# Optimization experiments

Measured on AMD Instinct MI355X. Metric: run time of the kernel, lower is better.

The kernel has to match this reference:

```python
import jax, jax.numpy as jnp
import numpy as np

ALPHA = 0.2          # LeakyReLU negative slope
NEG_INF = -9e15      # mask value used by the original module


def setup_inputs() -> dict:
    key = jax.random.key(0)
    k1, k2, k3, k4 = jax.random.split(key, 4)
    N, C, F, H, E = 4096, 512, 64, 8, 131072
    x = jax.random.normal(k1, (N, C), dtype=jnp.float32)
    edge_index = jax.random.randint(k2, (2, E), 0, N, dtype=jnp.int64)
    # xavier_uniform with gain=1.414 (per-head params stacked on leading axis)
    lim_W = 1.414 * np.sqrt(6.0 / (C + F))
    lim_a = 1.414 * np.sqrt(6.0 / (2 * F + 1))
    W = jax.random.uniform(k3, (H, C, F), minval=-lim_W, maxval=lim_W, dtype=jnp.float32)
    a = jax.random.uniform(k4, (H, 2 * F, 1), minval=-lim_a, maxval=lim_a, dtype=jnp.float32)
    return {"x": x, "edge_index": edge_index, "W": W, "a": a}


def reference(x, edge_index, W, a):
    # x: [N, C]; edge_index: [2, E]; W: [H, C, F]; a: [H, 2F, 1]
    N = x.shape[0]
    H, C, F = W.shape
    # dense adjacency with self-loops (duplicate edges collapse to True, matching adj > 0)
    adj = jnp.zeros((N, N), dtype=bool).at[edge_index[0], edge_index[1]].set(True)
    diag = jnp.arange(N)
    adj = adj.at[diag, diag].set(True)
    # per-head projection: h[h_, i] = x_i @ W[h_]
    h = jnp.einsum('nc,hcf->hnf', x, W)                       # [H, N, F]
    # e_ij = leakyrelu(h_i . a[:F] + h_j . a[F:]) -- identical math to the
    # original's NxN pairwise concat, without materializing [N*N, 2F]
    a_src = a[:, :F, 0]                                        # [H, F]
    a_dst = a[:, F:, 0]                                        # [H, F]
    s_src = jnp.einsum('hnf,hf->hn', h, a_src)                 # [H, N]
    s_dst = jnp.einsum('hnf,hf->hn', h, a_dst)                 # [H, N]
    e = s_src[:, :, None] + s_dst[:, None, :]                  # [H, N, N]
    e = jnp.where(e > 0, e, ALPHA * e)                         # LeakyReLU
    e = jnp.where(adj[None, :, :], e, NEG_INF)                 # mask non-edges
    att = jax.nn.softmax(e, axis=-1)                           # row softmax (dropout=0 / eval)
    out = jnp.einsum('hij,hjf->hif', att, h)                   # [H, N, F]
    out = jnp.transpose(out, (1, 0, 2)).reshape(N, H * F)      # concat heads
    return jax.nn.softmax(out, axis=1)
```

## Files before the change

kernel.cpp:

```cpp
#include <hip/hip_runtime.h>

#define ALPHA 0.2f

typedef __attribute__((ext_vector_type(8))) short short8;
typedef __attribute__((ext_vector_type(8))) unsigned short ushort8;
typedef __attribute__((ext_vector_type(4))) float f32x4;

__device__ __forceinline__ float bf2f(unsigned short u) {
    return __uint_as_float(((unsigned int)u) << 16);
}
__device__ __forceinline__ unsigned short f2bf(float f) {
    unsigned int x = __float_as_uint(f);
    unsigned int r = (x + 0x7fffu + ((x >> 16) & 1u)) >> 16;
    return (unsigned short)r;
}

__device__ __forceinline__ int detect_is32(const unsigned int* xw) {
    int lane = threadIdx.x & 63;
    unsigned int u = xw[lane];
    unsigned int e = (u >> 7) & 0xffu;
    unsigned long long b = __ballot(e >= 0x58u && e <= 0x90u);
    return (__popcll(b) < 40) ? 1 : 0;
}

__global__ __launch_bounds__(256) void split_bf16(const void* __restrict__ x_raw,
                                                  const void* __restrict__ W_raw,
                                                  unsigned short* __restrict__ x_hi,
                                                  unsigned short* __restrict__ x_lo,
                                                  unsigned short* __restrict__ wt_hi,
                                                  unsigned short* __restrict__ wt_lo,
                                                  int* __restrict__ flags) {
    int bid = blockIdx.x, tid = threadIdx.x;
    int is32 = detect_is32((const unsigned int*)x_raw);
    if (bid == 0 && tid == 0) flags[0] = is32;

    if (bid < 1024) {
        size_t base = ((size_t)bid * 256 + tid) * 8;
        ushort8 h8, l8;
        if (is32) {
            const float* xf = (const float*)x_raw;
            float4 v0 = *(const float4*)(xf + base);
            float4 v1 = *(const float4*)(xf + base + 4);
            float v[8] = {v0.x, v0.y, v0.z, v0.w, v1.x, v1.y, v1.z, v1.w};
#pragma unroll
            for (int j = 0; j < 8; j++) {
                unsigned short hi = f2bf(v[j]);
                h8[j] = hi;
                l8[j] = f2bf(v[j] - bf2f(hi));
            }
        } else {
            const ushort8* xb = (const ushort8*)x_raw;
            h8 = xb[base / 8];
            l8 = (ushort8)0;
        }
        *(ushort8*)(x_hi + base) = h8;
        *(ushort8*)(x_lo + base) = l8;
    } else {
        size_t u = ((size_t)(bid - 1024) * 256 + tid) * 8;
#pragma unroll
        for (int j = 0; j < 8; j++) {
            size_t e = u + j;
            int head = (int)(e >> 15);
            int c = (int)((e >> 6) & 511);
            int f = (int)(e & 63);
            unsigned short hi, lo;
            if (is32) {
                float v = ((const float*)W_raw)[e];
                hi = f2bf(v);
                lo = f2bf(v - bf2f(hi));
            } else {
                hi = ((const unsigned short*)W_raw)[e];
                lo = 0;
            }
            size_t o = (size_t)head * 32768 + (size_t)f * 512 + c;
            wt_hi[o] = hi;
            wt_lo[o] = lo;
        }
    }
}

__global__ __launch_bounds__(256) void build_adj(const int* __restrict__ ei, int E, int N,
                                                 unsigned long long* __restrict__ adj) {
    int lane = threadIdx.x & 63;
    unsigned long long nz = __ballot(ei[2 * lane + 1] != 0);
    int is64 = (nz == 0ull) ? 1 : 0;

    int t = blockIdx.x * blockDim.x + threadIdx.x;
    int words = N >> 6;
    if (t < E) {
        int r = is64 ? ei[2 * t]       : ei[t];
        int c = is64 ? ei[2 * (E + t)] : ei[E + t];
        atomicOr(&adj[(size_t)r * words + (c >> 6)], 1ull << (c & 63));
    } else if (t < E + N) {
        int i = t - E;
        atomicOr(&adj[(size_t)i * words + (i >> 6)], 1ull << (i & 63));
    }
}

#define LROW 72
__global__ __launch_bounds__(256) void gemm_mfma(const unsigned short* __restrict__ xh,
                                                 const unsigned short* __restrict__ xl,
                                                 const unsigned short* __restrict__ wth,
                                                 const unsigned short* __restrict__ wtl,
                                                 const void* __restrict__ a_raw,
                                                 unsigned short* __restrict__ h2b,
                                                 float* __restrict__ s_src2,
                                                 float* __restrict__ s_dst2,
                                                 const int* __restrict__ flags) {
    __shared__ unsigned short sA[2][64 * LROW];
    __shared__ unsigned short sB[2][64 * LROW];

    int head = blockIdx.y;
    int row0 = blockIdx.x * 64;
    int tid = threadIdx.x;
    int w = tid >> 6, lane = tid & 63;
    int m = lane & 15, quad = lane >> 4;
    int srow = tid >> 2, sc = tid & 3;

    const unsigned short* Ap[3] = {xh, xl, xh};
    const unsigned short* Bp[3] = {wth, wth, wtl};
    size_t baseA = (size_t)(row0 + srow) * 512 + sc * 8;
    size_t baseB = (size_t)head * 32768 + (size_t)srow * 512 + sc * 8;

    int ldsw  = srow * LROW + sc * 8;
    int ldsAr = (w * 16 + m) * LROW + quad * 8;

    f32x4 acc[4] = {f32x4{0.f, 0.f, 0.f, 0.f}, f32x4{0.f, 0.f, 0.f, 0.f},
                    f32x4{0.f, 0.f, 0.f, 0.f}, f32x4{0.f, 0.f, 0.f, 0.f}};

#define LOADSET(Aa, Ab, Ba, Bb, c)                                         \
    {                                                                      \
        const unsigned short* pA = Ap[(c) >> 3];                           \
        const unsigned short* pB = Bp[(c) >> 3];                           \
        size_t ko = (size_t)((c) & 7) * 64;                                \
        Aa = *(const ushort8*)(pA + baseA + ko);                           \
        Ab = *(const ushort8*)(pA + baseA + ko + 32);                      \
        Ba = *(const ushort8*)(pB + baseB + ko);                           \
        Bb = *(const ushort8*)(pB + baseB + ko + 32);                      \
    }

#define WRITESET(buf, Aa, Ab, Ba, Bb)                                      \
    {                                                                      \
        *(ushort8*)&sA[buf][ldsw]      = Aa;                               \
        *(ushort8*)&sA[buf][ldsw + 32] = Ab;                               \
        *(ushort8*)&sB[buf][ldsw]      = Ba;                               \
        *(ushort8*)&sB[buf][ldsw + 32] = Bb;                               \
    }

#define COMPUTE(buf)                                                       \
    {                                                                      \
        short8 af0 = *(const short8*)&sA[buf][ldsAr];                      \
        short8 af1 = *(const short8*)&sA[buf][ldsAr + 32];                 \
        _Pragma("unroll")                                                  \
        for (int t = 0; t < 4; t++) {                                      \
            int bo = (t * 16 + m) * LROW + quad * 8;                       \
            short8 bf0 = *(const short8*)&sB[buf][bo];                     \
            short8 bf1 = *(const short8*)&sB[buf][bo + 32];                \
            acc[t] = __builtin_amdgcn_mfma_f32_16x16x32_bf16(af0, bf0, acc[t], 0, 0, 0); \
            acc[t] = __builtin_amdgcn_mfma_f32_16x16x32_bf16(af1, bf1, acc[t], 0, 0, 0); \
        }                                                                  \
    }

    ushort8 a0a, a0b, b0a, b0b;
    ushort8 a1a, a1b, b1a, b1b;

    LOADSET(a0a, a0b, b0a, b0b, 0)
    LOADSET(a1a, a1b, b1a, b1b, 1)
    WRITESET(0, a0a, a0b, b0a, b0b)
    __syncthreads();

    for (int i = 0; i < 24; i += 2) {
        if (i + 2 < 24) LOADSET(a0a, a0b, b0a, b0b, i + 2)
        COMPUTE(0)
        WRITESET(1, a1a, a1b, b1a, b1b)
        __syncthreads();
        if (i + 3 < 24) LOADSET(a1a, a1b, b1a, b1b, i + 3)
        COMPUTE(1)
        if (i + 2 < 24) WRITESET(0, a0a, a0b, b0a, b0b)
        __syncthreads();
    }

#pragma unroll
    for (int t = 0; t < 4; t++)
#pragma unroll
        for (int reg = 0; reg < 4; reg++) {
            int r = row0 + w * 16 + quad * 4 + reg;
            h2b[(size_t)r * 512 + head * 64 + t * 16 + m] = f2bf(acc[t][reg]);
        }

    float as[4], ad[4];
    if (flags[0]) {
        const float* af32 = (const float*)a_raw + head * 128;
#pragma unroll
        for (int t = 0; t < 4; t++) {
            as[t] = af32[t * 16 + m];
            ad[t] = af32[64 + t * 16 + m];
        }
    } else {
        const unsigned short* ab = (const unsigned short*)a_raw + head * 128;
#pragma unroll
        for (int t = 0; t < 4; t++) {
            as[t] = bf2f(ab[t * 16 + m]);
            ad[t] = bf2f(ab[64 + t * 16 + m]);
        }
    }
#pragma unroll
    for (int reg = 0; reg < 4; reg++) {
        float s1 = as[0] * acc[0][reg] + as[1] * acc[1][reg] + as[2] * acc[2][reg] + as[3] * acc[3][reg];
        float s2 = ad[0] * acc[0][reg] + ad[1] * acc[1][reg] + ad[2] * acc[2][reg] + ad[3] * acc[3][reg];
#pragma unroll
        for (int d = 1; d < 16; d <<= 1) {
            s1 += __shfl_xor(s1, d);
            s2 += __shfl_xor(s2, d);
        }
        if (m == 0) {
            int r = row0 + w * 16 + quad * 4 + reg;
            s_src2[(size_t)r * 8 + head] = s1;
            s_dst2[(size_t)r * 8 + head] = s2;
        }
    }
}

__global__ __launch_bounds__(256) void attn_out(const unsigned short* __restrict__ h2b,
                                                const float* __restrict__ s_src2,
                                                const float* __restrict__ s_dst2,
                                                const unsigned long long* __restrict__ adj,
                                                void* __restrict__ out_raw,
                                                const int* __restrict__ flags) {
    __shared__ unsigned short nbrs[4096];
    __shared__ float w_lds[256 * 8];
    __shared__ float sss[8], smax[8], sden[8];
    __shared__ float sredw[4][8];
    __shared__ float sr[8];
    __shared__ int s_cnt;

    int i = blockIdx.x;
    int tid = threadIdx.x;
    int lane = tid & 63, wid = tid >> 6;

    if (tid < 64) {
        unsigned long long word = adj[(size_t)i * 64 + tid];
        int cnt = __popcll(word);
        int incl = cnt;
#pragma unroll
        for (int d = 1; d < 64; d <<= 1) {
            int v = __shfl_up(incl, d);
            if (tid >= d) incl += v;
        }
        int off = incl - cnt;
        unsigned long long w = word;
        int base = tid * 64;
        while (w) {
            int b = __ffsll((unsigned long long)w) - 1;
            nbrs[off++] = (unsigned short)(base + b);
            w &= w - 1;
        }
        if (tid == 63) s_cnt = incl;
    }
    if (tid >= 64 && tid < 72) sss[tid - 64] = s_src2[(size_t)i * 8 + (tid - 64)];
    __syncthreads();
    int cnt = s_cnt;

    int hw = tid & 7;
    float mp = -1e30f;
    for (int t = tid; t < cnt * 8; t += 256)
        mp = fmaxf(mp, s_dst2[(size_t)nbrs[t >> 3] * 8 + hw]);
    mp = fmaxf(mp, __shfl_down(mp, 32));
    mp = fmaxf(mp, __shfl_down(mp, 16));
    mp = fmaxf(mp, __shfl_down(mp, 8));
    if (lane < 8) sredw[wid][lane] = mp;
    __syncthreads();
    if (tid < 8) {
        float m = fmaxf(fmaxf(sredw[0][tid], sredw[1][tid]), fmaxf(sredw[2][tid], sredw[3][tid]));
        float pre = sss[tid] + m;
        smax[tid] = pre > 0.f ? pre : ALPHA * pre;
    }
    __syncthreads();

    int hh = tid >> 5;
    float ssrc_w = sss[hw], maxe_w = smax[hw];
    float den = 0.f, ax = 0.f, ay = 0.f;
    for (int c0 = 0; c0 < cnt; c0 += 256) {
        int csz = min(256, cnt - c0);
        __syncthreads();
        for (int t = tid; t < csz * 8; t += 256) {
            int j = nbrs[c0 + (t >> 3)];
            float e = ssrc_w + s_dst2[(size_t)j * 8 + hw];
            e = e > 0.f ? e : ALPHA * e;
            float w = __expf(e - maxe_w);
            w_lds[t] = w;
            den += w;
        }
        __syncthreads();
#pragma unroll 2
        for (int jj = 0; jj < csz; jj++) {
            int j = nbrs[c0 + jj];
            unsigned int u = *(const unsigned int*)(h2b + (size_t)j * 512 + tid * 2);
            float w = w_lds[jj * 8 + hh];
            ax += w * bf2f((unsigned short)(u & 0xffffu));
            ay += w * bf2f((unsigned short)(u >> 16));
        }
    }

    den += __shfl_down(den, 32);
    den += __shfl_down(den, 16);
    den += __shfl_down(den, 8);
    if (lane < 8) sredw[wid][lane] = den;
    __syncthreads();
    if (tid < 8) sden[tid] = sredw[0][tid] + sredw[1][tid] + sredw[2][tid] + sredw[3][tid];
    __syncthreads();
    float dtot = sden[hh];
    float o0 = ax / dtot, o1 = ay / dtot;

    float m2 = fmaxf(o0, o1);
#pragma unroll
    for (int d = 32; d; d >>= 1) m2 = fmaxf(m2, __shfl_down(m2, d));
    if (lane == 0) sr[wid] = m2;
    __syncthreads();
    float m = fmaxf(fmaxf(sr[0], sr[1]), fmaxf(sr[2], sr[3]));
    float e0 = __expf(o0 - m), e1 = __expf(o1 - m);
    float s = e0 + e1;
#pragma unroll
    for (int d = 32; d; d >>= 1) s += __shfl_down(s, d);
    __syncthreads();
    if (lane == 0) sr[wid + 4] = s;
    __syncthreads();
    s = sr[4] + sr[5] + sr[6] + sr[7];

    if (flags[0]) {
        float2* out = (float2*)out_raw;
        out[(size_t)i * 256 + tid] = make_float2(e0 / s, e1 / s);
    } else {
        unsigned int* out = (unsigned int*)out_raw;
        out[(size_t)i * 256 + tid] = (unsigned int)f2bf(e0 / s) | ((unsigned int)f2bf(e1 / s) << 16);
    }
}

extern "C" void kernel_launch(void* const* d_in, const int* in_sizes, int n_in,
                              void* d_out, int out_size, void* d_ws, size_t ws_size,
                              hipStream_t stream) {
    const int N = 4096, H = 8;
    const int E = in_sizes[1] / 2;

    const void* x = d_in[0];
    const int*  ei = (const int*)d_in[1];
    const void* W = d_in[2];
    const void* a = d_in[3];

    char* ws = (char*)d_ws;
    unsigned short* h2b = (unsigned short*)ws;
    float* s_src2 = (float*)(ws + (size_t)4 * 1024 * 1024);
    float* s_dst2 = s_src2 + (size_t)N * H;
    unsigned long long* adj = (unsigned long long*)(ws + (size_t)5 * 1024 * 1024);
    int* flags = (int*)(ws + (size_t)7 * 1024 * 1024 + 512 * 1024);
    unsigned short* x_hi  = (unsigned short*)(ws + (size_t)8 * 1024 * 1024);
    unsigned short* x_lo  = (unsigned short*)(ws + (size_t)12 * 1024 * 1024);
    unsigned short* wt_hi = (unsigned short*)(ws + (size_t)16 * 1024 * 1024);
    unsigned short* wt_lo = (unsigned short*)(ws + (size_t)16 * 1024 * 1024 + 512 * 1024);

    hipMemsetAsync(adj, 0, (size_t)N * (N / 8), stream);

    split_bf16<<<1152, 256, 0, stream>>>(x, W, x_hi, x_lo, wt_hi, wt_lo, flags);
    build_adj<<<(E + N + 255) / 256, 256, 0, stream>>>(ei, E, N, adj);
    gemm_mfma<<<dim3(N / 64, H), 256, 0, stream>>>(x_hi, x_lo, wt_hi, wt_lo, a,
                                                   h2b, s_src2, s_dst2, flags);
    attn_out<<<N, 256, 0, stream>>>(h2b, s_src2, s_dst2, adj, d_out, flags);
}
```

Baseline: 118.7 us.

## Split GEMM K across waves with 64x64 per-wave tiles; use global max for softmax

The GEMM now gives each wave a full 64x64 output tile over a quarter of the K chunks, with per-wave LDS buffers and no block barriers in the main loop. The partial tiles are reduced through LDS at the end, and the attention scores are computed from the reduced tile. The per-row neighbour max pass in attn_out is replaced by a per-head global max of s_dst, gathered with an encoded atomicMax in the GEMM epilogue. This removes a gather pass and two barriers per row. The cost is a looser softmax shift, which is mathematically valid but could hurt numerical range, plus extra registers and LDS in the GEMM.

```diff
diff --git a/kernel.cpp b/kernel.cpp
--- a/kernel.cpp
+++ b/kernel.cpp
@@ -13,6 +13,14 @@
     unsigned int x = __float_as_uint(f);
     unsigned int r = (x + 0x7fffu + ((x >> 16) & 1u)) >> 16;
     return (unsigned short)r;
+}
+__device__ __forceinline__ unsigned int encf(float f) {
+    int i = __float_as_int(f);
+    return (unsigned int)(i ^ ((i >> 31) | 0x80000000));
+}
+__device__ __forceinline__ float decf(unsigned int u) {
+    int i = (int)((u & 0x80000000u) ? (u ^ 0x80000000u) : ~u);
+    return __int_as_float(i);
 }
 
 __device__ __forceinline__ int detect_is32(const unsigned int* xw) {
@@ -33,6 +41,7 @@
     int bid = blockIdx.x, tid = threadIdx.x;
     int is32 = detect_is32((const unsigned int*)x_raw);
     if (bid == 0 && tid == 0) flags[0] = is32;
+    if (bid == 0 && tid >= 8 && tid < 16) flags[tid] = 0;
 
     if (bid < 1024) {
         size_t base = ((size_t)bid * 256 + tid) * 8;
@@ -97,128 +106,144 @@
     }
 }
 
-#define LROW 72
-__global__ __launch_bounds__(256) void gemm_mfma(const unsigned short* __restrict__ xh,
-                                                 const unsigned short* __restrict__ xl,
-                                                 const unsigned short* __restrict__ wth,
-                                                 const unsigned short* __restrict__ wtl,
-                                                 const void* __restrict__ a_raw,
-                                                 unsigned short* __restrict__ h2b,
-                                                 float* __restrict__ s_src2,
-                                                 float* __restrict__ s_dst2,
-                                                 const int* __restrict__ flags) {
-    __shared__ unsigned short sA[2][64 * LROW];
-    __shared__ unsigned short sB[2][64 * LROW];
+#define LR 36
+__global__ __launch_bounds__(256, 2) void gemm_mfma(const unsigned short* __restrict__ xh,
+                                                    const unsigned short* __restrict__ xl,
+                                                    const unsigned short* __restrict__ wth,
+                                                    const unsigned short* __restrict__ wtl,
+                                                    const void* __restrict__ a_raw,
+                                                    unsigned short* __restrict__ h2b,
+                                                    float* __restrict__ s_src2,
+                                                    float* __restrict__ s_dst2,
+                                                    int* __restrict__ flags) {
+    __shared__ unsigned short sbuf[4][2][2][64 * LR];
 
     int head = blockIdx.y;
     int row0 = blockIdx.x * 64;
     int tid = threadIdx.x;
     int w = tid >> 6, lane = tid & 63;
     int m = lane & 15, quad = lane >> 4;
-    int srow = tid >> 2, sc = tid & 3;
+    int srow = lane >> 2, skc = lane & 3;
+    size_t wbase = (size_t)head * 32768;
 
     const unsigned short* Ap[3] = {xh, xl, xh};
     const unsigned short* Bp[3] = {wth, wth, wtl};
-    size_t baseA = (size_t)(row0 + srow) * 512 + sc * 8;
-    size_t baseB = (size_t)head * 32768 + (size_t)srow * 512 + sc * 8;
-
-    int ldsw  = srow * LROW + sc * 8;
-    int ldsAr = (w * 16 + m) * LROW + quad * 8;
-
-    f32x4 acc[4] = {f32x4{0.f, 0.f, 0.f, 0.f}, f32x4{0.f, 0.f, 0.f, 0.f},
-                    f32x4{0.f, 0.f, 0.f, 0.f}, f32x4{0.f, 0.f, 0.f, 0.f}};
-
-#define LOADSET(Aa, Ab, Ba, Bb, c)                                         \
-    {                                                                      \
-        const unsigned short* pA = Ap[(c) >> 3];                           \
-        const unsigned short* pB = Bp[(c) >> 3];                           \
-        size_t ko = (size_t)((c) & 7) * 64;                                \
-        Aa = *(const ushort8*)(pA + baseA + ko);                           \
-        Ab = *(const ushort8*)(pA + baseA + ko + 32);                      \
-        Ba = *(const ushort8*)(pB + baseB + ko);                           \
-        Bb = *(const ushort8*)(pB + baseB + ko + 32);                      \
-    }
-
-#define WRITESET(buf, Aa, Ab, Ba, Bb)                                      \
-    {                                                                      \
-        *(ushort8*)&sA[buf][ldsw]      = Aa;                               \
-        *(ushort8*)&sA[buf][ldsw + 32] = Ab;                               \
-        *(ushort8*)&sB[buf][ldsw]      = Ba;                               \
-        *(ushort8*)&sB[buf][ldsw + 32] = Bb;                               \
-    }
-
-#define COMPUTE(buf)                                                       \
-    {                                                                      \
-        short8 af0 = *(const short8*)&sA[buf][ldsAr];                      \
-        short8 af1 = *(const short8*)&sA[buf][ldsAr + 32];                 \
-        _Pragma("unroll")                                                  \
-        for (int t = 0; t < 4; t++) {                                      \
-            int bo = (t * 16 + m) * LROW + quad * 8;                       \
-            short8 bf0 = *(const short8*)&sB[buf][bo];                     \
-            short8 bf1 = *(const short8*)&sB[buf][bo + 32];                \
-            acc[t] = __builtin_amdgcn_mfma_f32_16x16x32_bf16(af0, bf0, acc[t], 0, 0, 0); \
-            acc[t] = __builtin_amdgcn_mfma_f32_16x16x32_bf16(af1, bf1, acc[t], 0, 0, 0); \
-        }                                                                  \
-    }
-
-    ushort8 a0a, a0b, b0a, b0b;
-    ushort8 a1a, a1b, b1a, b1b;
-
-    LOADSET(a0a, a0b, b0a, b0b, 0)
-    LOADSET(a1a, a1b, b1a, b1b, 1)
-    WRITESET(0, a0a, a0b, b0a, b0b)
-    __syncthreads();
-
-    for (int i = 0; i < 24; i += 2) {
-        if (i + 2 < 24) LOADSET(a0a, a0b, b0a, b0b, i + 2)
-        COMPUTE(0)
-        WRITESET(1, a1a, a1b, b1a, b1b)
-        __syncthreads();
-        if (i + 3 < 24) LOADSET(a1a, a1b, b1a, b1b, i + 3)
-        COMPUTE(1)
-        if (i + 2 < 24) WRITESET(0, a0a, a0b, b0a, b0b)
-        __syncthreads();
-    }
-
-#pragma unroll
-    for (int t = 0; t < 4; t++)
-#pragma unroll
-        for (int reg = 0; reg < 4; reg++) {
-            int r = row0 + w * 16 + quad * 4 + reg;
-            h2b[(size_t)r * 512 + head * 64 + t * 16 + m] = f2bf(acc[t][reg]);
-        }
-
-    float as[4], ad[4];
+
+    f32x4 acc[4][4];
+#pragma unroll
+    for (int a = 0; a < 4; a++)
+#pragma unroll
+        for (int b = 0; b < 4; b++) acc[a][b] = f32x4{0.f, 0.f, 0.f, 0.f};
+
+#define LOADC(RA, RB, c)                                                        \
+    {                                                                           \
+        const unsigned short* pA = Ap[(c) >> 4];                                \
+        const unsigned short* pB = Bp[(c) >> 4];                                \
+        size_t ko = (size_t)((c) & 15) * 32;                                    \
+        _Pragma("unroll")                                                       \
+        for (int p = 0; p < 4; p++) {                                           \
+            RA[p] = *(const ushort8*)(pA + (size_t)(row0 + p * 16 + srow) * 512 + ko + skc * 8); \
+            RB[p] = *(const ushort8*)(pB + wbase + (size_t)(p * 16 + srow) * 512 + ko + skc * 8); \
+        }                                                                       \
+    }
+
+#define WRITEC(buf, RA, RB)                                                     \
+    {                                                                           \
+        _Pragma("unroll")                                                       \
+        for (int p = 0; p < 4; p++) {                                           \
+            *(ushort8*)&sbuf[w][buf][0][(p * 16 + srow) * LR + skc * 8] = RA[p]; \
+            *(ushort8*)&sbuf[w][buf][1][(p * 16 + srow) * LR + skc * 8] = RB[p]; \
+        }                                                                       \
+    }
+
+#define COMPUTEC(buf)                                                           \
+    {                                                                           \
+        short8 af[4], bfr[4];                                                   \
+        _Pragma("unroll")                                                       \
+        for (int t = 0; t < 4; t++) {                                           \
+            af[t]  = *(const short8*)&sbuf[w][buf][0][(t * 16 + m) * LR + quad * 8]; \
+            bfr[t] = *(const short8*)&sbuf[w][buf][1][(t * 16 + m) * LR + quad * 8]; \
+        }                                                                       \
+        _Pragma("unroll")                                                       \
+        for (int mt = 0; mt < 4; mt++)                                          \
+            _Pragma("unroll")                                                   \
+            for (int nt = 0; nt < 4; nt++)                                      \
+                acc[mt][nt] = __builtin_amdgcn_mfma_f32_16x16x32_bf16(af[mt], bfr[nt], acc[mt][nt], 0, 0, 0); \
+    }
+
+    int c0 = w * 12;
+    ushort8 eA[4], eB[4], oA[4], oB[4];
+    LOADC(eA, eB, c0)
+    LOADC(oA, oB, c0 + 1)
+    WRITEC(0, eA, eB)
+
+    for (int ci = 0; ci < 12; ci += 2) {
+        if (ci + 2 < 12) LOADC(eA, eB, c0 + ci + 2)
+        COMPUTEC(0)
+        WRITEC(1, oA, oB)
+        if (ci + 3 < 12) LOADC(oA, oB, c0 + ci + 3)
+        COMPUTEC(1)
+        if (ci + 2 < 12) WRITEC(0, eA, eB)
+    }
+
+    float* sp = (float*)&sbuf[0][0][0][0];
+    __syncthreads();
+#pragma unroll
+    for (int mt = 0; mt < 4; mt++)
+#pragma unroll
+        for (int nt = 0; nt < 4; nt++)
+#pragma unroll
+            for (int reg = 0; reg < 4; reg++) {
+                int row = mt * 16 + quad * 4 + reg;
+                sp[w * 4096 + row * 64 + nt * 16 + m] = acc[mt][nt][reg];
+            }
+    __syncthreads();
+
+    int r = tid >> 2, cc = tid & 3;
+    float c16[16];
+#pragma unroll
+    for (int i = 0; i < 16; i++) c16[i] = 0.f;
+#pragma unroll
+    for (int g = 0; g < 4; g++) {
+        const float* q = sp + g * 4096 + r * 64 + cc * 16;
+#pragma unroll
+        for (int v = 0; v < 4; v++) {
+            float4 f = *(const float4*)(q + v * 4);
+            c16[v * 4 + 0] += f.x; c16[v * 4 + 1] += f.y;
+            c16[v * 4 + 2] += f.z; c16[v * 4 + 3] += f.w;
+        }
+    }
+
+    ushort8 pk0, pk1;
+#pragma unroll
+    for (int i = 0; i < 8; i++) { pk0[i] = f2bf(c16[i]); pk1[i] = f2bf(c16[8 + i]); }
+    unsigned short* hb = h2b + (size_t)(row0 + r) * 512 + head * 64 + cc * 16;
+    *(ushort8*)hb = pk0;
+    *(ushort8*)(hb + 8) = pk1;
+
+    float as[16], ad[16];
     if (flags[0]) {
-        const float* af32 = (const float*)a_raw + head * 128;
-#pragma unroll
-        for (int t = 0; t < 4; t++) {
-            as[t] = af32[t * 16 + m];
-            ad[t] = af32[64 + t * 16 + m];
-        }
+        const float* af = (const float*)a_raw + head * 128 + cc * 16;
+#pragma unroll
+        for (int i = 0; i < 16; i++) { as[i] = af[i]; ad[i] = af[64 + i]; }
     } else {
-        const unsigned short* ab = (const unsigned short*)a_raw + head * 128;
-#pragma unroll
-        for (int t = 0; t < 4; t++) {
-            as[t] = bf2f(ab[t * 16 + m]);
-            ad[t] = bf2f(ab[64 + t * 16 + m]);
-        }
-    }
-#pragma unroll
-    for (int reg = 0; reg < 4; reg++) {
-        float s1 = as[0] * acc[0][reg] + as[1] * acc[1][reg] + as[2] * acc[2][reg] + as[3] * acc[3][reg];
-        float s2 = ad[0] * acc[0][reg] + ad[1] * acc[1][reg] + ad[2] * acc[2][reg] + ad[3] * acc[3][reg];
-#pragma unroll
-        for (int d = 1; d < 16; d <<= 1) {
-            s1 += __shfl_xor(s1, d);
-            s2 += __shfl_xor(s2, d);
-        }
-        if (m == 0) {
-            int r = row0 + w * 16 + quad * 4 + reg;
-            s_src2[(size_t)r * 8 + head] = s1;
-            s_dst2[(size_t)r * 8 + head] = s2;
-        }
-    }
+        const unsigned short* ab = (const unsigned short*)a_raw + head * 128 + cc * 16;
+#pragma unroll
+        for (int i = 0; i < 16; i++) { as[i] = bf2f(ab[i]); ad[i] = bf2f(ab[64 + i]); }
+    }
+    float s1 = 0.f, s2 = 0.f;
+#pragma unroll
+    for (int i = 0; i < 16; i++) { s1 += c16[i] * as[i]; s2 += c16[i] * ad[i]; }
+    s1 += __shfl_xor(s1, 1); s1 += __shfl_xor(s1, 2);
+    s2 += __shfl_xor(s2, 1); s2 += __shfl_xor(s2, 2);
+    if ((tid & 3) == 0) {
+        s_src2[(size_t)(row0 + r) * 8 + head] = s1;
+        s_dst2[(size_t)(row0 + r) * 8 + head] = s2;
+    }
+    float gm = s2;
+#pragma unroll
+    for (int d = 4; d < 64; d <<= 1) gm = fmaxf(gm, __shfl_xor(gm, d));
+    if (lane == 0) atomicMax((unsigned int*)&flags[8 + head], encf(gm));
 }
 
 __global__ __launch_bounds__(256) void attn_out(const unsigned short* __restrict__ h2b,
@@ -257,26 +282,17 @@
         }
         if (tid == 63) s_cnt = incl;
     }
-    if (tid >= 64 && tid < 72) sss[tid - 64] = s_src2[(size_t)i * 8 + (tid - 64)];
+    if (tid >= 64 && tid < 72) {
+        int h = tid - 64;
+        float ss = s_src2[(size_t)i * 8 + h];
+        sss[h] = ss;
+        float pre = ss + decf((unsigned int)flags[8 + h]);
+        smax[h] = pre > 0.f ? pre : ALPHA * pre;
+    }
     __syncthreads();
     int cnt = s_cnt;
 
     int hw = tid & 7;
-    float mp = -1e30f;
-    for (int t = tid; t < cnt * 8; t += 256)
-        mp = fmaxf(mp, s_dst2[(size_t)nbrs[t >> 3] * 8 + hw]);
-    mp = fmaxf(mp, __shfl_down(mp, 32));
-    mp = fmaxf(mp, __shfl_down(mp, 16));
-    mp = fmaxf(mp, __shfl_down(mp, 8));
-    if (lane < 8) sredw[wid][lane] = mp;
-    __syncthreads();
-    if (tid < 8) {
-        float m = fmaxf(fmaxf(sredw[0][tid], sredw[1][tid]), fmaxf(sredw[2][tid], sredw[3][tid]));
-        float pre = sss[tid] + m;
-        smax[tid] = pre > 0.f ? pre : ALPHA * pre;
-    }
-    __syncthreads();
-
     int hh = tid >> 5;
     float ssrc_w = sss[hw], maxe_w = smax[hw];
     float den = 0.f, ax = 0.f, ay = 0.f;
```

Result: slower. 136.6 us (+15.1%).

## Use global per-head s_dst max for softmax shift; batch neighbor gathers by eight

Applied to the files above, without the earlier changes.

The gemm kernel now reduces the per-head maximum of s_dst and publishes it through an order-preserving atomicMax into the flags buffer. attn_out uses that global maximum as the softmax shift, which removes the per-row neighbor max pass and two block barriers. The aggregation loop is also unrolled so that eight h2b row loads are issued before they are consumed, which raises memory-level parallelism. The global shift is looser than the per-row maximum, so rows whose neighbors sit far below it could underflow in exp. The new flag slots also depend on being zeroed in the earlier split kernel on every call.

```diff
diff --git a/kernel.cpp b/kernel.cpp
--- a/kernel.cpp
+++ b/kernel.cpp
@@ -13,6 +13,14 @@
     unsigned int x = __float_as_uint(f);
     unsigned int r = (x + 0x7fffu + ((x >> 16) & 1u)) >> 16;
     return (unsigned short)r;
+}
+__device__ __forceinline__ unsigned int encf(float f) {
+    int i = __float_as_int(f);
+    return (unsigned int)(i ^ ((i >> 31) | 0x80000000));
+}
+__device__ __forceinline__ float decf(unsigned int u) {
+    int i = (int)((u & 0x80000000u) ? (u ^ 0x80000000u) : ~u);
+    return __int_as_float(i);
 }
 
 __device__ __forceinline__ int detect_is32(const unsigned int* xw) {
@@ -33,6 +41,7 @@
     int bid = blockIdx.x, tid = threadIdx.x;
     int is32 = detect_is32((const unsigned int*)x_raw);
     if (bid == 0 && tid == 0) flags[0] = is32;
+    if (bid == 0 && tid >= 8 && tid < 16) flags[tid] = 0;
 
     if (bid < 1024) {
         size_t base = ((size_t)bid * 256 + tid) * 8;
@@ -106,7 +115,7 @@
                                                  unsigned short* __restrict__ h2b,
                                                  float* __restrict__ s_src2,
                                                  float* __restrict__ s_dst2,
-                                                 const int* __restrict__ flags) {
+                                                 int* __restrict__ flags) {
     __shared__ unsigned short sA[2][64 * LROW];
     __shared__ unsigned short sB[2][64 * LROW];
 
@@ -204,6 +213,7 @@
             ad[t] = bf2f(ab[64 + t * 16 + m]);
         }
     }
+    float gmax = -1e30f;
 #pragma unroll
     for (int reg = 0; reg < 4; reg++) {
         float s1 = as[0] * acc[0][reg] + as[1] * acc[1][reg] + as[2] * acc[2][reg] + as[3] * acc[3][reg];
@@ -213,12 +223,16 @@
             s1 += __shfl_xor(s1, d);
             s2 += __shfl_xor(s2, d);
         }
+        gmax = fmaxf(gmax, s2);
         if (m == 0) {
             int r = row0 + w * 16 + quad * 4 + reg;
             s_src2[(size_t)r * 8 + head] = s1;
             s_dst2[(size_t)r * 8 + head] = s2;
         }
     }
+#pragma unroll
+    for (int d = 16; d < 64; d <<= 1) gmax = fmaxf(gmax, __shfl_xor(gmax, d));
+    if (lane == 0) atomicMax((unsigned int*)&flags[8 + head], encf(gmax));
 }
 
 __global__ __launch_bounds__(256) void attn_out(const unsigned short* __restrict__ h2b,
@@ -257,26 +271,17 @@
         }
         if (tid == 63) s_cnt = incl;
     }
-    if (tid >= 64 && tid < 72) sss[tid - 64] = s_src2[(size_t)i * 8 + (tid - 64)];
+    if (tid >= 64 && tid < 72) {
+        int h = tid - 64;
+        float ss = s_src2[(size_t)i * 8 + h];
+        sss[h] = ss;
+        float pre = ss + decf((unsigned int)flags[8 + h]);
+        smax[h] = pre > 0.f ? pre : ALPHA * pre;
+    }
     __syncthreads();
     int cnt = s_cnt;
 
     int hw = tid & 7;
-    float mp = -1e30f;
-    for (int t = tid; t < cnt * 8; t += 256)
-        mp = fmaxf(mp, s_dst2[(size_t)nbrs[t >> 3] * 8 + hw]);
-    mp = fmaxf(mp, __shfl_down(mp, 32));
-    mp = fmaxf(mp, __shfl_down(mp, 16));
-    mp = fmaxf(mp, __shfl_down(mp, 8));
-    if (lane < 8) sredw[wid][lane] = mp;
-    __syncthreads();
-    if (tid < 8) {
-        float m = fmaxf(fmaxf(sredw[0][tid], sredw[1][tid]), fmaxf(sredw[2][tid], sredw[3][tid]));
-        float pre = sss[tid] + m;
-        smax[tid] = pre > 0.f ? pre : ALPHA * pre;
-    }
-    __syncthreads();
-
     int hh = tid >> 5;
     float ssrc_w = sss[hw], maxe_w = smax[hw];
     float den = 0.f, ax = 0.f, ay = 0.f;
@@ -292,8 +297,23 @@
             den += w;
         }
         __syncthreads();
-#pragma unroll 2
-        for (int jj = 0; jj < csz; jj++) {
+
+        int jj = 0;
+        for (; jj + 8 <= csz; jj += 8) {
+            int j[8]; unsigned int u[8]; float wv[8];
+#pragma unroll
+            for (int k = 0; k < 8; k++) j[k] = nbrs[c0 + jj + k];
+#pragma unroll
+            for (int k = 0; k < 8; k++) u[k] = *(const unsigned int*)(h2b + (size_t)j[k] * 512 + tid * 2);
+#pragma unroll
+            for (int k = 0; k < 8; k++) wv[k] = w_lds[(jj + k) * 8 + hh];
+#pragma unroll
+            for (int k = 0; k < 8; k++) {
+                ax += wv[k] * bf2f((unsigned short)(u[k] & 0xffffu));
+                ay += wv[k] * bf2f((unsigned short)(u[k] >> 16));
+            }
+        }
+        for (; jj < csz; jj++) {
             int j = nbrs[c0 + jj];
             unsigned int u = *(const unsigned int*)(h2b + (size_t)j * 512 + tid * 2);
             float w = w_lds[jj * 8 + hh];
```

New measurement: 133.1 us. 12.1% more time.
